# Kernel tuning notes

Hardware: AMD Instinct MI355X
Metric: run time of the kernel (lower is better)

## Reference

```python
import jax, jax.numpy as jnp
import numpy as np

HID = 256
STYLE_DIM = 64
NUM_STYLES = 8
IN_DIM = 3 + STYLE_DIM


def setup_inputs() -> dict:
    key = jax.random.key(0)
    ks = jax.random.split(key, 12)
    B, H, W = 2, 512, 512
    rgb = jax.random.uniform(ks[0], (B, 3, H, W), dtype=jnp.float32)
    style_idx = jax.random.randint(ks[1], (B,), 0, NUM_STYLES, dtype=jnp.int32)
    # style embedding table (torch init: normal std=0.01)
    emb_table = 0.01 * jax.random.normal(ks[2], (NUM_STYLES, STYLE_DIM), dtype=jnp.float32)
    # kaiming-normal (fan_in, relu gain sqrt(2)) weights stored as [in, out]
    def kaiming(k, fan_in, fan_out):
        std = np.sqrt(2.0 / fan_in)
        return std * jax.random.normal(k, (fan_in, fan_out), dtype=jnp.float32)
    W0 = kaiming(ks[3], IN_DIM, HID); b0 = jnp.zeros((HID,), jnp.float32)
    W1 = kaiming(ks[4], HID, HID);    b1 = jnp.zeros((HID,), jnp.float32)
    W2 = kaiming(ks[5], HID, HID);    b2 = jnp.zeros((HID,), jnp.float32)
    W3 = kaiming(ks[6], HID, 3);      b3 = jnp.zeros((3,), jnp.float32)
    return {"rgb": rgb, "style_idx": style_idx, "emb_table": emb_table,
            "W0": W0, "b0": b0, "W1": W1, "b1": b1,
            "W2": W2, "b2": b2, "W3": W3, "b3": b3}


def reference(rgb, style_idx, emb_table, W0, b0, W1, b1, W2, b2, W3, b3):
    B, C, H, W_ = rgb.shape  # CHW image input
    # [B,3,H,W] -> [B*H*W, 3]
    rgb_flat = jnp.transpose(rgb, (0, 2, 3, 1)).reshape(-1, 3)
    # style embedding lookup, broadcast per pixel
    emb = emb_table[style_idx]                              # [B, style_dim]
    emb = jnp.broadcast_to(emb[:, None, :], (B, H * W_, STYLE_DIM)).reshape(-1, STYLE_DIM)
    x = jnp.concatenate([rgb_flat, emb], axis=-1)           # [N, 67]
    gelu = lambda t: jax.nn.gelu(t, approximate=False)      # torch nn.GELU default (erf)
    x = gelu(x @ W0 + b0)
    x = gelu(x @ W1 + b1)
    x = gelu(x @ W2 + b2)
    out_flat = jax.nn.sigmoid(x @ W3 + b3)                  # [N, 3]
    out = out_flat.reshape(B, H, W_, 3).transpose(0, 3, 1, 2)
    return out
```

## Files before the change

kernel.cpp:

```cpp
#include <hip/hip_runtime.h>

#define HW  (512*512)

typedef _Float16 half8 __attribute__((__vector_size__(16)));
typedef float    floatx4 __attribute__((__vector_size__(16)));

__device__ __forceinline__ float gelu_f(float x){
    float x2 = x * x;
    float q  = __builtin_fmaf(x2, -0.1029432f, -2.3022079f);
    float e  = __builtin_amdgcn_exp2f(x * q);
    return x * __builtin_amdgcn_rcpf(1.0f + e);
}

__device__ __forceinline__ float sigmoid_f(float x){
    float e = __builtin_amdgcn_exp2f(-1.44269504f * x);
    return __builtin_amdgcn_rcpf(1.0f + e);
}

__global__ void pack_w(const float* __restrict__ W1, const float* __restrict__ W2,
                       const float* __restrict__ W3, _Float16* __restrict__ wp){
    int gid = blockIdx.x * 256 + threadIdx.x;
    if (gid >= 135168) return;
    if (gid < 131072){
        int i    = gid & 65535;
        int j    = i & 7;
        int lane = (i >> 3) & 63;
        int blk  = i >> 9;
        int ks = blk >> 4, nt = blk & 15;
        int k = ks*32 + ((lane >> 4) << 3) + j;
        int n = nt*16 + (lane & 15);
        const float* W = (gid < 65536) ? W1 : W2;
        wp[gid] = (_Float16)W[k*256 + n];
    } else {
        int i    = gid - 131072;
        int j    = i & 7;
        int lane = (i >> 3) & 63;
        int ks   = i >> 9;
        int k = ks*32 + ((lane >> 4) << 3) + j;
        int n = lane & 15;
        wp[gid] = (_Float16)((n < 3) ? W3[k*3 + n] : 0.0f);
    }
}

__global__ void prep_c0(const float* __restrict__ emb, const int* __restrict__ sidx,
                        const float* __restrict__ W0, const float* __restrict__ b0,
                        float* __restrict__ c0){
    int n = threadIdx.x;
    int b = blockIdx.x;
    int s = sidx[b];
    float acc = b0[n];
    #pragma unroll 8
    for (int d = 0; d < 64; d++)
        acc = fmaf(emb[s*64 + d], W0[(3 + d)*256 + n], acc);
    c0[b*256 + n] = acc;
}

__global__ __launch_bounds__(256, 2)
void nilut_main(const float* __restrict__ rgb,
                const float* __restrict__ W0,
                const float* __restrict__ b1v,
                const float* __restrict__ b2v,
                const float* __restrict__ b3v,
                const _Float16* __restrict__ wp,
                const float* __restrict__ c0,
                float* __restrict__ out){
    __shared__ __align__(16) _Float16 act[128 * 264];
    __shared__ __align__(16) float    w0s[1024];

    const int tid = threadIdx.x;
    const int wg  = blockIdx.x;
    const int pixbase = wg * 128;
    const int b   = pixbase >> 18;
    const int hw0 = pixbase & (HW - 1);

    #pragma unroll
    for (int r = 0; r < 4; r++){
        int q = r*256 + tid;
        w0s[q] = (q < 768) ? W0[q] : c0[b*256 + (q - 768)];
    }
    __syncthreads();

    {
        int row  = tid & 127;
        int half = tid >> 7;
        int base = b*3*HW + hw0 + row;
        float rr = rgb[base], gg = rgb[base + HW], bb = rgb[base + 2*HW];
        #pragma unroll
        for (int cg = 0; cg < 16; cg++){
            int nc = half*128 + cg*8;
            half8 v;
            #pragma unroll
            for (int j = 0; j < 8; j++){
                int n = nc + j;
                float z = fmaf(rr, w0s[n], fmaf(gg, w0s[256 + n], fmaf(bb, w0s[512 + n], w0s[768 + n])));
                v[j] = (_Float16)gelu_f(z);
            }
            *(half8*)&act[row*264 + nc] = v;
        }
    }
    __syncthreads();

    const int lane = tid & 63;
    const int wv   = tid >> 6;
    const int ln15 = lane & 15;
    const int q8   = (lane >> 4) * 8;
    const int qr   = (lane >> 4) * 4;

    const _Float16* wl  = wp;
    const float* bias   = b1v;
    #pragma unroll 1
    for (int L = 0; L < 2; L++){
        const int mh = wv >> 1, nh = wv & 1;
        const int rbase = mh * 64;
        const int cb16  = nh * 8;
        floatx4 acc[4][8];
        #pragma unroll
        for (int m = 0; m < 4; m++)
            #pragma unroll
            for (int nt = 0; nt < 8; nt++)
                acc[m][nt] = (floatx4){0.f, 0.f, 0.f, 0.f};

        const half8* wp8 = (const half8*)wl;
        #pragma unroll 2
        for (int ks = 0; ks < 8; ks++){
            half8 a[4];
            #pragma unroll
            for (int m = 0; m < 4; m++)
                a[m] = *(const half8*)&act[(rbase + m*16 + ln15)*264 + ks*32 + q8];
            #pragma unroll
            for (int nt = 0; nt < 8; nt++){
                half8 bf = wp8[(ks*16 + cb16 + nt)*64 + lane];
                #pragma unroll
                for (int m = 0; m < 4; m++)
                    acc[m][nt] = __builtin_amdgcn_mfma_f32_16x16x32_f16(a[m], bf, acc[m][nt], 0, 0, 0);
            }
        }
        __syncthreads();
        #pragma unroll
        for (int nt = 0; nt < 8; nt++){
            int n = (cb16 + nt)*16 + ln15;
            float bv = bias[n];
            #pragma unroll
            for (int m = 0; m < 4; m++){
                #pragma unroll
                for (int r = 0; r < 4; r++){
                    int row = rbase + m*16 + qr + r;
                    float x = acc[m][nt][r] + bv;
                    act[row*264 + n] = (_Float16)gelu_f(x);
                }
            }
        }
        __syncthreads();
        wl = wp + 65536;
        bias = b2v;
    }

    {
        const half8* wp8 = (const half8*)(wp + 131072);
        int rbase = wv * 32;
        floatx4 a0c = (floatx4){0.f,0.f,0.f,0.f};
        floatx4 a1c = (floatx4){0.f,0.f,0.f,0.f};
        #pragma unroll
        for (int ks = 0; ks < 8; ks++){
            half8 a0 = *(const half8*)&act[(rbase + ln15)*264 + ks*32 + q8];
            half8 a1 = *(const half8*)&act[(rbase + 16 + ln15)*264 + ks*32 + q8];
            half8 bf = wp8[ks*64 + lane];
            a0c = __builtin_amdgcn_mfma_f32_16x16x32_f16(a0, bf, a0c, 0, 0, 0);
            a1c = __builtin_amdgcn_mfma_f32_16x16x32_f16(a1, bf, a1c, 0, 0, 0);
        }
        if (ln15 < 3){
            float bv = b3v[ln15];
            #pragma unroll
            for (int r = 0; r < 4; r++){
                int row0 = rbase + qr + r;
                w0s[ln15*128 + row0]      = sigmoid_f(a0c[r] + bv);
                w0s[ln15*128 + row0 + 16] = sigmoid_f(a1c[r] + bv);
            }
        }
        __syncthreads();
        if (tid < 96){
            int c  = tid >> 5;
            int i2 = tid & 31;
            float4* dst = (float4*)(out + (b*3 + c)*HW + hw0);
            dst[i2] = ((float4*)(w0s + c*128))[i2];
        }
    }
}

extern "C" void kernel_launch(void* const* d_in, const int* in_sizes, int n_in,
                              void* d_out, int out_size, void* d_ws, size_t ws_size,
                              hipStream_t stream){
    const float* rgb = (const float*)d_in[0];
    const int*  sidx = (const int*) d_in[1];
    const float* emb = (const float*)d_in[2];
    const float* W0  = (const float*)d_in[3];
    const float* b0  = (const float*)d_in[4];
    const float* W1  = (const float*)d_in[5];
    const float* b1  = (const float*)d_in[6];
    const float* W2  = (const float*)d_in[7];
    const float* b2  = (const float*)d_in[8];
    const float* W3  = (const float*)d_in[9];
    const float* b3  = (const float*)d_in[10];
    float* out = (float*)d_out;

    _Float16* wp = (_Float16*)d_ws;
    float*    c0 = (float*)((char*)d_ws + 270336);

    int n_pix = in_sizes[0] / 3;
    pack_w <<<528, 256, 0, stream>>>(W1, W2, W3, wp);
    prep_c0<<<2,   256, 0, stream>>>(emb, sidx, W0, b0, c0);
    nilut_main<<<n_pix / 128, 256, 0, stream>>>(rgb, W0, b1, b2, b3, wp, c0, out);
}
```

Measured before the change: 300.3 us.

## Use 512-thread blocks, XOR-swizzled LDS activations, fold bias, merge prep kernels

The main kernel now runs 8 waves per 128-pixel tile instead of 4, so each wave owns 64x64 outputs instead of 64x128. That halves accumulator registers and lets more waves run per CU. The padded LDS activation layout (stride 264) is replaced by an unpadded stride-256 layout with an XOR swizzle, which shrinks shared memory while trying to keep bank conflicts away. Bias is loaded into the accumulator init, and the two setup kernels are merged into one launch. The risks are the extra swizzle index math and more block-level synchronisation across 8 waves.

```diff
diff --git a/kernel.cpp b/kernel.cpp
--- a/kernel.cpp
+++ b/kernel.cpp
@@ -17,45 +17,50 @@
     return __builtin_amdgcn_rcpf(1.0f + e);
 }
 
-__global__ void pack_w(const float* __restrict__ W1, const float* __restrict__ W2,
-                       const float* __restrict__ W3, _Float16* __restrict__ wp){
-    int gid = blockIdx.x * 256 + threadIdx.x;
-    if (gid >= 135168) return;
-    if (gid < 131072){
-        int i    = gid & 65535;
-        int j    = i & 7;
-        int lane = (i >> 3) & 63;
-        int blk  = i >> 9;
-        int ks = blk >> 4, nt = blk & 15;
-        int k = ks*32 + ((lane >> 4) << 3) + j;
-        int n = nt*16 + (lane & 15);
-        const float* W = (gid < 65536) ? W1 : W2;
-        wp[gid] = (_Float16)W[k*256 + n];
+__device__ __forceinline__ int swz(int row){
+    return ((row & 3) << 3) ^ (((row >> 2) & 3) << 4);
+}
+
+__global__ void prep_all(const float* __restrict__ W1, const float* __restrict__ W2,
+                         const float* __restrict__ W3, const float* __restrict__ emb,
+                         const int* __restrict__ sidx, const float* __restrict__ W0,
+                         const float* __restrict__ b0,
+                         _Float16* __restrict__ wp, float* __restrict__ c0){
+    int blk = blockIdx.x;
+    int tid = threadIdx.x;
+    if (blk < 528){
+        int gid = blk * 256 + tid;
+        if (gid < 131072){
+            int i    = gid & 65535;
+            int j    = i & 7;
+            int lane = (i >> 3) & 63;
+            int b2   = i >> 9;
+            int ks = b2 >> 4, nt = b2 & 15;
+            int k = ks*32 + ((lane >> 4) << 3) + j;
+            int n = nt*16 + (lane & 15);
+            const float* W = (gid < 65536) ? W1 : W2;
+            wp[gid] = (_Float16)W[k*256 + n];
+        } else {
+            int i    = gid - 131072;
+            int j    = i & 7;
+            int lane = (i >> 3) & 63;
+            int ks   = i >> 9;
+            int k = ks*32 + ((lane >> 4) << 3) + j;
+            int n = lane & 15;
+            wp[gid] = (_Float16)((n < 3) ? W3[k*3 + n] : 0.0f);
+        }
     } else {
-        int i    = gid - 131072;
-        int j    = i & 7;
-        int lane = (i >> 3) & 63;
-        int ks   = i >> 9;
-        int k = ks*32 + ((lane >> 4) << 3) + j;
-        int n = lane & 15;
-        wp[gid] = (_Float16)((n < 3) ? W3[k*3 + n] : 0.0f);
-    }
-}
-
-__global__ void prep_c0(const float* __restrict__ emb, const int* __restrict__ sidx,
-                        const float* __restrict__ W0, const float* __restrict__ b0,
-                        float* __restrict__ c0){
-    int n = threadIdx.x;
-    int b = blockIdx.x;
-    int s = sidx[b];
-    float acc = b0[n];
-    #pragma unroll 8
-    for (int d = 0; d < 64; d++)
-        acc = fmaf(emb[s*64 + d], W0[(3 + d)*256 + n], acc);
-    c0[b*256 + n] = acc;
-}
-
-__global__ __launch_bounds__(256, 2)
+        int b = blk - 528;
+        int s = sidx[b];
+        float acc = b0[tid];
+        #pragma unroll 8
+        for (int d = 0; d < 64; d++)
+            acc = fmaf(emb[s*64 + d], W0[(3 + d)*256 + tid], acc);
+        c0[b*256 + tid] = acc;
+    }
+}
+
+__global__ __launch_bounds__(512, 4)
 void nilut_main(const float* __restrict__ rgb,
                 const float* __restrict__ W0,
                 const float* __restrict__ b1v,
@@ -64,7 +69,7 @@
                 const _Float16* __restrict__ wp,
                 const float* __restrict__ c0,
                 float* __restrict__ out){
-    __shared__ __align__(16) _Float16 act[128 * 264];
+    __shared__ __align__(16) _Float16 act[128 * 256];
     __shared__ __align__(16) float    w0s[1024];
 
     const int tid = threadIdx.x;
@@ -74,20 +79,21 @@
     const int hw0 = pixbase & (HW - 1);
 
     #pragma unroll
-    for (int r = 0; r < 4; r++){
-        int q = r*256 + tid;
+    for (int r = 0; r < 2; r++){
+        int q = r*512 + tid;
         w0s[q] = (q < 768) ? W0[q] : c0[b*256 + (q - 768)];
     }
     __syncthreads();
 
     {
-        int row  = tid & 127;
-        int half = tid >> 7;
+        int row = tid & 127;
+        int ch  = tid >> 7;
+        int sr  = swz(row);
         int base = b*3*HW + hw0 + row;
         float rr = rgb[base], gg = rgb[base + HW], bb = rgb[base + 2*HW];
         #pragma unroll
-        for (int cg = 0; cg < 16; cg++){
-            int nc = half*128 + cg*8;
+        for (int cg = 0; cg < 8; cg++){
+            int nc = ch*64 + cg*8;
             half8 v;
             #pragma unroll
             for (int j = 0; j < 8; j++){
@@ -95,7 +101,7 @@
                 float z = fmaf(rr, w0s[n], fmaf(gg, w0s[256 + n], fmaf(bb, w0s[512 + n], w0s[768 + n])));
                 v[j] = (_Float16)gelu_f(z);
             }
-            *(half8*)&act[row*264 + nc] = v;
+            *(half8*)&act[row*256 + (nc ^ sr)] = v;
         }
     }
     __syncthreads();
@@ -103,32 +109,37 @@
     const int lane = tid & 63;
     const int wv   = tid >> 6;
     const int ln15 = lane & 15;
-    const int q8   = (lane >> 4) * 8;
-    const int qr   = (lane >> 4) * 4;
+    const int quad = lane >> 4;
+    const int q8   = quad * 8;
+    const int qr   = quad * 4;
+    const int sA   = swz(ln15);
 
     const _Float16* wl  = wp;
     const float* bias   = b1v;
+    const int mh = wv >> 2, nh = wv & 3;
+    const int rbase = mh * 64;
+    const int cb16  = nh * 4;
     #pragma unroll 1
     for (int L = 0; L < 2; L++){
-        const int mh = wv >> 1, nh = wv & 1;
-        const int rbase = mh * 64;
-        const int cb16  = nh * 8;
-        floatx4 acc[4][8];
-        #pragma unroll
-        for (int m = 0; m < 4; m++)
-            #pragma unroll
-            for (int nt = 0; nt < 8; nt++)
-                acc[m][nt] = (floatx4){0.f, 0.f, 0.f, 0.f};
+        floatx4 acc[4][4];
+        #pragma unroll
+        for (int nt = 0; nt < 4; nt++){
+            float bv = bias[(cb16 + nt)*16 + ln15];
+            #pragma unroll
+            for (int m = 0; m < 4; m++)
+                acc[m][nt] = (floatx4){bv, bv, bv, bv};
+        }
 
         const half8* wp8 = (const half8*)wl;
         #pragma unroll 2
         for (int ks = 0; ks < 8; ks++){
+            int k0 = (ks*32 + q8) ^ sA;
             half8 a[4];
             #pragma unroll
             for (int m = 0; m < 4; m++)
-                a[m] = *(const half8*)&act[(rbase + m*16 + ln15)*264 + ks*32 + q8];
-            #pragma unroll
-            for (int nt = 0; nt < 8; nt++){
+                a[m] = *(const half8*)&act[(rbase + m*16 + ln15)*256 + k0];
+            #pragma unroll
+            for (int nt = 0; nt < 4; nt++){
                 half8 bf = wp8[(ks*16 + cb16 + nt)*64 + lane];
                 #pragma unroll
                 for (int m = 0; m < 4; m++)
@@ -137,16 +148,15 @@
         }
         __syncthreads();
         #pragma unroll
-        for (int nt = 0; nt < 8; nt++){
+        for (int nt = 0; nt < 4; nt++){
             int n = (cb16 + nt)*16 + ln15;
-            float bv = bias[n];
             #pragma unroll
             for (int m = 0; m < 4; m++){
                 #pragma unroll
                 for (int r = 0; r < 4; r++){
                     int row = rbase + m*16 + qr + r;
-                    float x = acc[m][nt][r] + bv;
-                    act[row*264 + n] = (_Float16)gelu_f(x);
+                    int se  = (r << 3) ^ (quad << 4);
+                    act[row*256 + (n ^ se)] = (_Float16)gelu_f(acc[m][nt][r]);
                 }
             }
         }
@@ -157,24 +167,21 @@
 
     {
         const half8* wp8 = (const half8*)(wp + 131072);
-        int rbase = wv * 32;
-        floatx4 a0c = (floatx4){0.f,0.f,0.f,0.f};
-        floatx4 a1c = (floatx4){0.f,0.f,0.f,0.f};
+        int rbf = wv * 16;
+        floatx4 ac = (floatx4){0.f,0.f,0.f,0.f};
         #pragma unroll
         for (int ks = 0; ks < 8; ks++){
-            half8 a0 = *(const half8*)&act[(rbase + ln15)*264 + ks*32 + q8];
-            half8 a1 = *(const half8*)&act[(rbase + 16 + ln15)*264 + ks*32 + q8];
+            int k0 = (ks*32 + q8) ^ sA;
+            half8 a  = *(const half8*)&act[(rbf + ln15)*256 + k0];
             half8 bf = wp8[ks*64 + lane];
-            a0c = __builtin_amdgcn_mfma_f32_16x16x32_f16(a0, bf, a0c, 0, 0, 0);
-            a1c = __builtin_amdgcn_mfma_f32_16x16x32_f16(a1, bf, a1c, 0, 0, 0);
+            ac = __builtin_amdgcn_mfma_f32_16x16x32_f16(a, bf, ac, 0, 0, 0);
         }
         if (ln15 < 3){
             float bv = b3v[ln15];
             #pragma unroll
             for (int r = 0; r < 4; r++){
-                int row0 = rbase + qr + r;
-                w0s[ln15*128 + row0]      = sigmoid_f(a0c[r] + bv);
-                w0s[ln15*128 + row0 + 16] = sigmoid_f(a1c[r] + bv);
+                int row0 = rbf + qr + r;
+                w0s[ln15*128 + row0] = sigmoid_f(ac[r] + bv);
             }
         }
         __syncthreads();
@@ -207,7 +214,6 @@
     float*    c0 = (float*)((char*)d_ws + 270336);
 
     int n_pix = in_sizes[0] / 3;
-    pack_w <<<528, 256, 0, stream>>>(W1, W2, W3, wp);
-    prep_c0<<<2,   256, 0, stream>>>(emb, sidx, W0, b0, c0);
-    nilut_main<<<n_pix / 128, 256, 0, stream>>>(rgb, W0, b1, b2, b3, wp, c0, out);
-}
+    prep_all<<<530, 256, 0, stream>>>(W1, W2, W3, emb, sidx, W0, b0, wp, c0);
+    nilut_main<<<n_pix / 128, 512, 0, stream>>>(rgb, W0, b1, b2, b3, wp, c0, out);
+}
```

After: 288.0 us. 1.04x faster.
